# Kernel tuning notes

Measured on AMD Instinct MI355X. Metric: run time of the kernel, lower is better.

The kernel has to match this reference:

```python
import jax, jax.numpy as jnp
import numpy as np

H = 128   # hidden_dim
J = 24    # num_joints
L = 4     # num_layers
NH = 8    # attention heads
W = 120   # window
F = 256   # feedforward_size
D = 216   # input_dim (J * 9)
S = 60    # src len
T = 61    # tgt len (S+T-1 == W)
B = 2     # batch
HD = H // NH


def _ln(x, g, b, eps=1e-5):
    m = x.mean(-1, keepdims=True)
    v = ((x - m) ** 2).mean(-1, keepdims=True)
    return (x - m) / jnp.sqrt(v + eps) * g + b


def _mha(x, Wqkv, bqkv, Wo, bo, mask=None):
    # x: (seq, batch, H). torch MultiheadAttention with in_proj (3H,H), out_proj (H,H)
    s, bsz, _ = x.shape
    qkv = jnp.einsum('sbh,eh->sbe', x, Wqkv) + bqkv
    q, k, v = jnp.split(qkv, 3, axis=-1)
    q = q.reshape(s, bsz, NH, HD)
    k = k.reshape(s, bsz, NH, HD)
    v = v.reshape(s, bsz, NH, HD)
    scores = jnp.einsum('qbnd,kbnd->bnqk', q, k) * (1.0 / np.sqrt(HD))
    if mask is not None:
        scores = scores + mask
    a = jax.nn.softmax(scores, axis=-1)
    o = jnp.einsum('bnqk,kbnd->qbnd', a, v).reshape(s, bsz, H)
    return jnp.einsum('sbh,oh->sbo', o, Wo) + bo


def _make_pe(length, d):
    pos = np.arange(length)[:, None]
    div = np.exp(np.arange(0, d, 2) * (-np.log(10000.0) / d))
    pe = np.zeros((length, d), np.float32)
    pe[:, 0::2] = np.sin(pos * div)
    pe[:, 1::2] = np.cos(pos * div)
    return jnp.asarray(pe)


def setup_inputs() -> dict:
    key = jax.random.key(0)
    ks = jax.random.split(key, 16)
    def rn(i, shape, s=0.02):
        return jax.random.normal(ks[i], shape, dtype=jnp.float32) * s
    return {
        'src': rn(0, (B, S, D), 1.0),
        'tgt': rn(1, (B, T, D), 1.0),
        'Wemb': rn(2, (H * J, D)), 'bemb': jnp.zeros((H * J,), jnp.float32),
        'Wqkv_s': rn(3, (L, 3 * H, H)), 'bqkv_s': jnp.zeros((L, 3 * H), jnp.float32),
        'Wo_s': rn(4, (L, H, H)), 'bo_s': jnp.zeros((L, H), jnp.float32),
        'sn_g': jnp.ones((L, H), jnp.float32), 'sn_b': jnp.zeros((L, H), jnp.float32),
        'Wqkv_t': rn(5, (L, J, 3 * H, H)), 'bqkv_t': jnp.zeros((L, J, 3 * H), jnp.float32),
        'Wo_t': rn(6, (L, J, H, H)), 'bo_t': jnp.zeros((L, J, H), jnp.float32),
        'tn_g': jnp.ones((L, H), jnp.float32), 'tn_b': jnp.zeros((L, H), jnp.float32),
        'W1': rn(7, (L, F, H)), 'b1': jnp.zeros((L, F), jnp.float32),
        'W2': rn(8, (L, H, F)), 'b2': jnp.zeros((L, H), jnp.float32),
        'Wout': rn(9, (D // J, H)), 'bout': jnp.zeros((D // J,), jnp.float32),
    }


def _forward(src, tgt, Wemb, bemb, Wqkv_s, bqkv_s, Wo_s, bo_s, sn_g, sn_b,
             Wqkv_t, bqkv_t, Wo_t, bo_t, tn_g, tn_b, W1, b1, W2, b2, Wout, bout):
    src_ = src.swapaxes(0, 1)  # (S, B, D)
    tgt_ = tgt.swapaxes(0, 1)  # (T, B, D)
    concat = jnp.concatenate([src_, tgt_], axis=0)  # (W+1, B, D)
    total = concat.shape[0]
    max_len = total - 1  # == W
    emb = jnp.einsum('tbd,ed->tbe', concat, Wemb) + bemb
    emb = emb + _make_pe(total, H * J)[:, None, :]
    x0 = emb.reshape(total, concat.shape[1], J, H)
    # additive causal mask (original uses -inf; -1e9 is equivalent post-softmax)
    mask = jnp.asarray(np.where(np.tril(np.ones((W, W), bool)), 0.0, -1e9).astype(np.float32))
    tmha = jax.vmap(lambda xx, a, bb, c, dd: _mha(xx, a, bb, c, dd, mask))

    def layer(x, t, l):
        # spatial attention over joints at frame t
        sp = jnp.take(x, t, axis=0).transpose(1, 0, 2)  # (J, B, H)
        sa = _mha(sp, Wqkv_s[l], bqkv_s[l], Wo_s[l], bo_s[l])
        sp_out = _ln(sp + sa, sn_g[l], sn_b[l]).transpose(1, 0, 2)  # (B, J, H)
        # temporal attention per joint (distinct weights), causal over the window
        # since t < W always here, slice [max(0,t-W):max(t,W)] == [:W]
        temp = x[:W].transpose(2, 0, 1, 3)  # (J, W, B, H)
        ta = tmha(temp, Wqkv_t[l], bqkv_t[l], Wo_t[l], bo_t[l])
        tout = _ln(temp + ta, tn_g[l], tn_b[l]).transpose(1, 2, 0, 3)  # (W, B, J, H)
        tout = tout.at[t].add(sp_out)  # window_t = min(W-1, t) = t
        f = jax.nn.relu(jnp.einsum('wbjh,fh->wbjf', tout, W1[l]) + b1[l])
        f = 2.0 * f  # original: ffn = ffn + dropout(ffn); dropout is identity in eval
        return jnp.einsum('wbjf,hf->wbjh', f, W2[l]) + b2[l]

    def body(carry, t):
        x = x0
        for l in range(L):
            x = layer(x, t, l)
        proj = jnp.einsum('wbjh,oh->wbjo', x, Wout) + bout
        proj = proj.reshape(W, x.shape[1], D)
        out_t = jnp.take(proj, t, axis=0) + jnp.take(concat, t, axis=0)
        return carry, out_t

    _, outs = jax.lax.scan(body, None, jnp.arange(max_len))
    return outs.swapaxes(0, 1)  # (B, max_len, D)


def reference(src, tgt, Wemb, bemb, Wqkv_s, bqkv_s, Wo_s, bo_s, sn_g, sn_b,
              Wqkv_t, bqkv_t, Wo_t, bo_t, tn_g, tn_b, W1, b1, W2, b2, Wout, bout):
    return _forward(src, tgt, Wemb, bemb, Wqkv_s, bqkv_s, Wo_s, bo_s, sn_g, sn_b,
                    Wqkv_t, bqkv_t, Wo_t, bo_t, tn_g, tn_b, W1, b1, W2, b2, Wout, bout)
```

## Files before the change

kernel.cpp:

```cpp
#include <hip/hip_runtime.h>

#define TW 120
#define TB 2
#define TJ 24
#define TH 128
#define TNH 8
#define THD 16
#define TF 256
#define TD 216
#define TROWS (TW*TB*TJ)
#define TEMB (TJ*TH)
#define TBF 240
#define KPAD 256

#define QCH 60
#define LDT 136
#define SPAD (TH + 4)
#define HSEG (TW*THD)

typedef float f4 __attribute__((ext_vector_type(4)));
typedef short bf8 __attribute__((ext_vector_type(8)));
typedef short s4 __attribute__((ext_vector_type(4)));

__device__ __forceinline__ short f2bf(float x) {
    union { float f; unsigned u; } v; v.f = x;
    unsigned r = (v.u + 0x7FFFu + ((v.u >> 16) & 1u)) >> 16;
    return (short)r;
}

#define NW_QKV_S 196608
#define NW_O_S    65536
#define NW_QKV_T 4718592
#define NW_O_T   1572864
#define NW_1      131072
#define NW_2      131072
#define OFF_O_S   (NW_QKV_S)
#define OFF_QKV_T (OFF_O_S + NW_O_S)
#define OFF_O_T   (OFF_QKV_T + NW_QKV_T)
#define OFF_W1    (OFF_O_T + NW_O_T)
#define OFF_W2    (OFF_W1 + NW_1)
#define NW_TOT    (OFF_W2 + NW_2)
#define NB_CONV   (NW_TOT / 4 / 256)
#define NB_WEMB   (TEMB * KPAD / 4 / 256)
#define NB_CBUF   (TBF * KPAD / 4 / 256)

__global__ void convgather_kernel(const float* __restrict__ Wqkv_s, const float* __restrict__ Wo_s,
                                  const float* __restrict__ Wqkv_t, const float* __restrict__ Wo_t,
                                  const float* __restrict__ W1, const float* __restrict__ W2,
                                  short* __restrict__ dst,
                                  const float* __restrict__ Wemb, short* __restrict__ wembbf,
                                  const float* __restrict__ src, const float* __restrict__ tgt,
                                  short* __restrict__ cbufbf) {
    int bx = blockIdx.x, tid = threadIdx.x;
    if (bx < NB_CONV) {
        size_t i = ((size_t)bx * 256 + tid) * 4;
        const float* s; size_t off;
        if (i < NW_QKV_S)       { s = Wqkv_s; off = i; }
        else if (i < OFF_QKV_T) { s = Wo_s;   off = i - OFF_O_S; }
        else if (i < OFF_O_T)   { s = Wqkv_t; off = i - OFF_QKV_T; }
        else if (i < OFF_W1)    { s = Wo_t;   off = i - OFF_O_T; }
        else if (i < OFF_W2)    { s = W1;     off = i - OFF_W1; }
        else                    { s = W2;     off = i - OFF_W2; }
        f4 v = *(const f4*)(s + off);
        s4 o = { f2bf(v[0]), f2bf(v[1]), f2bf(v[2]), f2bf(v[3]) };
        *(s4*)(dst + i) = o;
    } else if (bx < NB_CONV + NB_WEMB) {
        int g = (bx - NB_CONV) * 256 + tid;
        int row = g >> 6;
        int colg = (g & 63) * 4;
        s4 o = {0, 0, 0, 0};
        if (colg < TD) {
            f4 v = *(const f4*)(Wemb + (size_t)row * TD + colg);
            o = { f2bf(v[0]), f2bf(v[1]), f2bf(v[2]), f2bf(v[3]) };
        }
        *(s4*)(wembbf + (size_t)row * KPAD + colg) = o;
    } else {
        int g = (bx - NB_CONV - NB_WEMB) * 256 + tid;
        int row = g >> 6;
        int colg = (g & 63) * 4;
        int b = row & 1, t = row >> 1;
        s4 o = {0, 0, 0, 0};
        if (colg < TD) {
            const float* sp = (t < 60) ? (src + ((size_t)b * 60 + t) * TD)
                                       : (tgt + ((size_t)b * 61 + (t - 60)) * TD);
            f4 v = *(const f4*)(sp + colg);
            o = { f2bf(v[0]), f2bf(v[1]), f2bf(v[2]), f2bf(v[3]) };
        }
        *(s4*)(cbufbf + (size_t)row * KPAD + colg) = o;
    }
}

__device__ __forceinline__ void stage_bf(short* Ds, const short* __restrict__ src,
                                         size_t rstride, int nrows, int tid) {
    int r = tid >> 2, s = (tid & 3) * 32;
    short* d = Ds + r * LDT + s;
    if (r < nrows) {
        const short* p = src + (size_t)r * rstride + s;
        *(bf8*)(d)      = *(const bf8*)(p);
        *(bf8*)(d + 8)  = *(const bf8*)(p + 8);
        *(bf8*)(d + 16) = *(const bf8*)(p + 16);
        *(bf8*)(d + 24) = *(const bf8*)(p + 24);
    } else {
        bf8 z = {0,0,0,0,0,0,0,0};
        *(bf8*)(d) = z; *(bf8*)(d+8) = z; *(bf8*)(d+16) = z; *(bf8*)(d+24) = z;
    }
}

__device__ __forceinline__ void mfma_tile64(const short* As, const short* Bs,
                                            int wave, int lane, f4 acc[2][2]) {
    int wm = wave >> 1, wn = wave & 1;
    int lrow = lane & 15, lk = (lane >> 4) * 8;
    #pragma unroll
    for (int ks = 0; ks < 4; ++ks) {
        bf8 a0 = *(const bf8*)&As[(wm*32      + lrow) * LDT + ks*32 + lk];
        bf8 a1 = *(const bf8*)&As[(wm*32 + 16 + lrow) * LDT + ks*32 + lk];
        bf8 b0 = *(const bf8*)&Bs[(wn*32      + lrow) * LDT + ks*32 + lk];
        bf8 b1 = *(const bf8*)&Bs[(wn*32 + 16 + lrow) * LDT + ks*32 + lk];
        acc[0][0] = __builtin_amdgcn_mfma_f32_16x16x32_bf16(a0, b0, acc[0][0], 0, 0, 0);
        acc[0][1] = __builtin_amdgcn_mfma_f32_16x16x32_bf16(a0, b1, acc[0][1], 0, 0, 0);
        acc[1][0] = __builtin_amdgcn_mfma_f32_16x16x32_bf16(a1, b0, acc[1][0], 0, 0, 0);
        acc[1][1] = __builtin_amdgcn_mfma_f32_16x16x32_bf16(a1, b1, acc[1][1], 0, 0, 0);
    }
}

__global__ __launch_bounds__(256) void mfma_embed_kernel(
        const short* __restrict__ cbufbf, const short* __restrict__ wembbf,
        const float* __restrict__ bemb, float* __restrict__ x0,
        short* __restrict__ x0bf, float* __restrict__ r0,
        short* __restrict__ r0bf) {
    __shared__ short As[64 * LDT], Bs[64 * LDT];
    int tid = threadIdx.x;
    int m0 = blockIdx.x * 64, n0 = blockIdx.y * 64;
    int mrem = TBF - m0; if (mrem > 64) mrem = 64;
    int wave = tid >> 6, lane = tid & 63;
    f4 acc[2][2] = {{{0,0,0,0},{0,0,0,0}},{{0,0,0,0},{0,0,0,0}}};
    #pragma unroll
    for (int kk = 0; kk < 2; ++kk) {
        stage_bf(As, cbufbf + (size_t)m0 * KPAD + kk * 128, KPAD, mrem, tid);
        stage_bf(Bs, wembbf + (size_t)n0 * KPAD + kk * 128, KPAD, 64, tid);
        __syncthreads();
        mfma_tile64(As, Bs, wave, lane, acc);
        __syncthreads();
    }
    int wm = wave >> 1, wn = wave & 1, lrow = lane & 15, gr = (lane >> 4) * 4;
    #pragma unroll
    for (int ni = 0; ni < 2; ++ni) {
        int col = n0 + wn*32 + ni*16 + lrow;
        float bv = bemb[col];
        float freq = expf((float)(col & ~1) * (-9.2103403719761836f / 3072.0f));
        float peodd = (col & 1) ? 1.f : 0.f;
        #pragma unroll
        for (int mi = 0; mi < 2; ++mi)
            #pragma unroll
            for (int rg = 0; rg < 4; ++rg) {
                int tr = wm*32 + mi*16 + gr + rg;
                if (tr < mrem) {
                    int grow = m0 + tr;
                    int t = grow >> 1;
                    float ang = (float)t * freq;
                    float pe = peodd ? cosf(ang) : sinf(ang);
                    float v = acc[mi][ni][rg] + bv + pe;
                    size_t off = (size_t)grow * TEMB + col;
                    x0[off] = v;
                    r0[off] = v;
                    short bvs = f2bf(v);
                    x0bf[off] = bvs;
                    r0bf[off] = bvs;
                }
            }
    }
}

__global__ __launch_bounds__(256) void mfma_qkvmega_kernel(
        const short* __restrict__ A2, const short* __restrict__ A3,
        const short* __restrict__ Wt, const short* __restrict__ Ws,
        const float* __restrict__ bt, const float* __restrict__ bs,
        float* __restrict__ Qp2, float* __restrict__ Kb2, float* __restrict__ Vb2,
        float* __restrict__ Qs_, float* __restrict__ Ks_, float* __restrict__ Vs_,
        float* __restrict__ Qt_, float* __restrict__ Kt_, float* __restrict__ Vt_,
        int p2n, int n0base) {
    __shared__ short As[64 * LDT], Bs[64 * LDT];
    int tid = threadIdx.x;
    int m0 = blockIdx.x * 64, j = blockIdx.z, yy = blockIdx.y;
    int mrem = TBF - m0; if (mrem > 64) mrem = 64;
    const short* Abf; const short* Wbf; const float* bias; int bofs, n0;
    float *dq, *dk, *dv;
    int headmajor;
    if (yy < p2n) {
        n0 = n0base + yy * 64;
        Abf = A2;
        Wbf = Wt + (size_t)j * 3 * TH * TH + (size_t)n0 * TH;
        bias = bt; bofs = j * 3 * TH;
        dq = Qp2; dk = Kb2; dv = Vb2;
        headmajor = 1;
    } else {
        int y2 = yy - p2n;
        int tmp = (y2 >= 6);
        n0 = (tmp ? y2 - 6 : y2) * 64;
        Abf = A3;
        if (tmp) { Wbf = Wt + (size_t)j * 3 * TH * TH + (size_t)n0 * TH; bias = bt; bofs = j * 3 * TH;
                   dq = Qt_; dk = Kt_; dv = Vt_; headmajor = 1; }
        else     { Wbf = Ws + (size_t)n0 * TH; bias = bs; bofs = 0;
                   dq = Qs_; dk = Ks_; dv = Vs_; headmajor = 0; }
    }
    stage_bf(As, Abf + (size_t)m0 * TEMB + j * TH, TEMB, mrem, tid);
    stage_bf(Bs, Wbf, TH, 64, tid);
    __syncthreads();
    int wave = tid >> 6, lane = tid & 63;
    f4 acc[2][2] = {{{0,0,0,0},{0,0,0,0}},{{0,0,0,0},{0,0,0,0}}};
    mfma_tile64(As, Bs, wave, lane, acc);
    int wm = wave >> 1, wn = wave & 1, lrow = lane & 15, gr = (lane >> 4) * 4;
    float* dst = (n0 < TH) ? dq : ((n0 < 2 * TH) ? dk : dv);
    int cb = n0 & (TH - 1);
    #pragma unroll
    for (int ni = 0; ni < 2; ++ni) {
        float bv = bias[bofs + n0 + wn*32 + ni*16 + lrow];
        int col = cb + wn*32 + ni*16 + lrow;
        #pragma unroll
        for (int mi = 0; mi < 2; ++mi)
            #pragma unroll
            for (int rg = 0; rg < 4; ++rg) {
                int tr = wm*32 + mi*16 + gr + rg;
                if (tr < mrem) {
                    int row = m0 + tr;
                    float v = acc[mi][ni][rg] + bv;
                    if (headmajor) {
                        int bb = row & 1, tt = row >> 1;
                        int hd = col >> 4, dd = col & 15;
                        dst[((size_t)((bb * TJ + j) * TNH + hd) * TW + tt) * THD + dd] = v;
                    } else {
                        dst[(size_t)(row * TJ + j) * TH + col] = v;
                    }
                }
            }
    }
}

__global__ __launch_bounds__(256) void attn_mega_kernel(
        const float* __restrict__ Qc_g, const float* __restrict__ Kc_g, const float* __restrict__ Vc_g,
        const float* __restrict__ Qs_g, const float* __restrict__ Ks_g, const float* __restrict__ Vs_g,
        const float* __restrict__ Qt_g, const float* __restrict__ Kt_g, const float* __restrict__ Vt_g,
        short* __restrict__ Oc, short* __restrict__ Os, short* __restrict__ Ot,
        int docausal) {
    __shared__ __align__(16) float smem[3 * TJ * SPAD];
    int bx = blockIdx.x;
    int tid = threadIdx.x;

    if (bx < 240) {
        float* Qs = smem;
        float* Ks = smem + TJ * SPAD;
        float* Vs = smem + 2 * TJ * SPAD;
        int b = bx & 1, t = bx >> 1;
        int base = (t * TB + b) * TJ;
        for (int i = tid; i < TJ * 32; i += 256) {
            int rr = i >> 5, c4 = i & 31;
            ((f4*)(Qs + rr * SPAD))[c4] = ((const f4*)(Qs_g + (size_t)(base + rr) * TH))[c4];
            ((f4*)(Ks + rr * SPAD))[c4] = ((const f4*)(Ks_g + (size_t)(base + rr) * TH))[c4];
            ((f4*)(Vs + rr * SPAD))[c4] = ((const f4*)(Vs_g + (size_t)(base + rr) * TH))[c4];
        }
        __syncthreads();
        if (tid >= 192) return;
        int qj = tid % TJ;
        int head = tid / TJ;
        int hb = head * THD;
        float qv[THD];
        #pragma unroll
        for (int u = 0; u < THD; ++u) qv[u] = Qs[qj * SPAD + hb + u];
        float sc[TJ];
        float m = -1e30f;
        #pragma unroll
        for (int k = 0; k < TJ; ++k) {
            float a = 0.f;
            #pragma unroll
            for (int u = 0; u < THD; ++u) a += qv[u] * Ks[k * SPAD + hb + u];
            sc[k] = a * 0.25f;
            m = fmaxf(m, sc[k]);
        }
        float sum = 0.f;
        #pragma unroll
        for (int k = 0; k < TJ; ++k) { sc[k] = __expf(sc[k] - m); sum += sc[k]; }
        float inv = 1.0f / sum;
        float o[THD];
        #pragma unroll
        for (int u = 0; u < THD; ++u) o[u] = 0.f;
        #pragma unroll
        for (int k = 0; k < TJ; ++k) {
            #pragma unroll
            for (int u = 0; u < THD; ++u) o[u] += sc[k] * Vs[k * SPAD + hb + u];
        }
        size_t off = (size_t)(base + qj) * TH + hb;
        #pragma unroll
        for (int u = 0; u < THD; ++u) Os[off + u] = f2bf(o[u] * inv);
        return;
    }

    int cx = bx - 240;
    int head = cx & 7;
    int j = (cx >> 3) % TJ;
    int b = (cx >> 3) / TJ;
    size_t base = (size_t)((b * TJ + j) * TNH + head) * HSEG;
    float* Kb = smem;
    float* Vb = smem + 1920;
    for (int i = tid; i < 480; i += 256) {
        ((f4*)Kb)[i] = ((const f4*)(Kc_g + base))[i];
        ((f4*)Vb)[i] = ((const f4*)(Vc_g + base))[i];
    }
    __syncthreads();
    int wave = tid >> 6, lane = tid & 63;
    int iscausal = (wave < 2);
    if (iscausal && !docausal) return;
    int qbase = (wave & 1) * 60;
    int act = (lane < 60);
    int q = qbase + (act ? lane : 59);
    const float* Qg = iscausal ? Qc_g : Qt_g;
    f4 Qr0 = *(const f4*)(Qg + base + (size_t)q * THD);
    f4 Qr1 = *(const f4*)(Qg + base + (size_t)q * THD + 4);
    f4 Qr2 = *(const f4*)(Qg + base + (size_t)q * THD + 8);
    f4 Qr3 = *(const f4*)(Qg + base + (size_t)q * THD + 12);
    f4 Ks0, Ks1, Ks2, Ks3, Vs0, Vs1, Vs2, Vs3;
    if (!iscausal) {
        Ks0 = *(const f4*)(Kt_g + base + (size_t)q * THD);
        Ks1 = *(const f4*)(Kt_g + base + (size_t)q * THD + 4);
        Ks2 = *(const f4*)(Kt_g + base + (size_t)q * THD + 8);
        Ks3 = *(const f4*)(Kt_g + base + (size_t)q * THD + 12);
        Vs0 = *(const f4*)(Vt_g + base + (size_t)q * THD);
        Vs1 = *(const f4*)(Vt_g + base + (size_t)q * THD + 4);
        Vs2 = *(const f4*)(Vt_g + base + (size_t)q * THD + 8);
        Vs3 = *(const f4*)(Vt_g + base + (size_t)q * THD + 12);
    }
    f4 a0 = {0,0,0,0}, a1 = {0,0,0,0}, a2 = {0,0,0,0}, a3 = {0,0,0,0};
    float sum = 0.f;
    int qc = iscausal ? q : (q - 1);
    int klim = qbase + 60;
    #pragma unroll 4
    for (int k = 0; k < klim; ++k) {
        const float* kr = Kb + k * 16;
        f4 d = Qr0 * ((const f4*)kr)[0] + Qr1 * ((const f4*)kr)[1]
             + Qr2 * ((const f4*)kr)[2] + Qr3 * ((const f4*)kr)[3];
        float s = (d[0] + d[1] + d[2] + d[3]) * 0.25f;
        float p = (k <= qc) ? __expf(s) : 0.f;
        sum += p;
        const float* vr = Vb + k * 16;
        a0 += p * ((const f4*)vr)[0];
        a1 += p * ((const f4*)vr)[1];
        a2 += p * ((const f4*)vr)[2];
        a3 += p * ((const f4*)vr)[3];
    }
    if (!iscausal) {
        f4 d = Qr0 * Ks0 + Qr1 * Ks1 + Qr2 * Ks2 + Qr3 * Ks3;
        float p = __expf((d[0] + d[1] + d[2] + d[3]) * 0.25f);
        sum += p;
        a0 += p * Vs0; a1 += p * Vs1; a2 += p * Vs2; a3 += p * Vs3;
    }
    if (act) {
        float inv = 1.0f / sum;
        short* O = iscausal ? Oc : Ot;
        size_t off = (size_t)((q * TB + b) * TJ + j) * TH + head * THD;
        s4 o0 = { f2bf(a0[0]*inv), f2bf(a0[1]*inv), f2bf(a0[2]*inv), f2bf(a0[3]*inv) };
        s4 o1 = { f2bf(a1[0]*inv), f2bf(a1[1]*inv), f2bf(a1[2]*inv), f2bf(a1[3]*inv) };
        s4 o2 = { f2bf(a2[0]*inv), f2bf(a2[1]*inv), f2bf(a2[2]*inv), f2bf(a2[3]*inv) };
        s4 o3 = { f2bf(a3[0]*inv), f2bf(a3[1]*inv), f2bf(a3[2]*inv), f2bf(a3[3]*inv) };
        *(s4*)(O + off)      = o0;
        *(s4*)(O + off + 4)  = o1;
        *(s4*)(O + off + 8)  = o2;
        *(s4*)(O + off + 12) = o3;
    }
}

__device__ __forceinline__ void oln_compute(
        const short* __restrict__ Abf, const short* __restrict__ Wbf,
        const float* __restrict__ bias, const float* __restrict__ resid,
        const float* __restrict__ g, const float* __restrict__ bln,
        int perJoint, int m0, int j,
        short* As, short* Bs, float* rsum, float* rsq, float* lnm, float* lnr,
        float o0[4], float o1[4]) {
    int tid = threadIdx.x;
    { int r = tid >> 4, s = (tid & 15) * 8;
      *(bf8*)&As[r * LDT + s] = *(const bf8*)(Abf + (size_t)(m0 + r) * TEMB + j * TH + s); }
    { int r = tid >> 1, s = (tid & 1) * 64;
      const short* p = Wbf + (perJoint ? (size_t)j * TH * TH : 0) + (size_t)r * TH + s;
      short* d = &Bs[r * LDT + s];
      #pragma unroll
      for (int cc = 0; cc < 64; cc += 8) *(bf8*)(d + cc) = *(const bf8*)(p + cc); }
    __syncthreads();
    int wave = tid >> 6, lane = tid & 63, lrow = lane & 15, lk = (lane >> 4) * 8, gr = (lane >> 4) * 4;
    f4 acc[2] = {{0,0,0,0},{0,0,0,0}};
    #pragma unroll
    for (int ks = 0; ks < 4; ++ks) {
        bf8 a  = *(const bf8*)&As[lrow * LDT + ks*32 + lk];
        bf8 b0 = *(const bf8*)&Bs[(wave*32      + lrow) * LDT + ks*32 + lk];
        bf8 b1 = *(const bf8*)&Bs[(wave*32 + 16 + lrow) * LDT + ks*32 + lk];
        acc[0] = __builtin_amdgcn_mfma_f32_16x16x32_bf16(a, b0, acc[0], 0, 0, 0);
        acc[1] = __builtin_amdgcn_mfma_f32_16x16x32_bf16(a, b1, acc[1], 0, 0, 0);
    }
    int col0 = wave*32 + lrow, col1 = col0 + 16;
    int bofs = perJoint ? j * TH : 0;
    float bv0 = bias[bofs + col0], bv1 = bias[bofs + col1];
    float v0[4], v1[4], sr_[4], sq_[4];
    #pragma unroll
    for (int rg = 0; rg < 4; ++rg) {
        size_t ro = (size_t)(m0 + gr + rg) * TEMB + j * TH;
        v0[rg] = acc[0][rg] + bv0 + resid[ro + col0];
        v1[rg] = acc[1][rg] + bv1 + resid[ro + col1];
        sr_[rg] = v0[rg] + v1[rg];
        sq_[rg] = v0[rg]*v0[rg] + v1[rg]*v1[rg];
    }
    #pragma unroll
    for (int o = 1; o < 16; o <<= 1) {
        #pragma unroll
        for (int rg = 0; rg < 4; ++rg) { sr_[rg] += __shfl_xor(sr_[rg], o); sq_[rg] += __shfl_xor(sq_[rg], o); }
    }
    if (lrow == 0) {
        #pragma unroll
        for (int rg = 0; rg < 4; ++rg) { rsum[wave*16 + gr + rg] = sr_[rg]; rsq[wave*16 + gr + rg] = sq_[rg]; }
    }
    __syncthreads();
    if (tid < 16) {
        float s = rsum[tid] + rsum[16 + tid] + rsum[32 + tid] + rsum[48 + tid];
        float q = rsq[tid] + rsq[16 + tid] + rsq[32 + tid] + rsq[48 + tid];
        float mean = s * (1.0f / TH);
        float var = q * (1.0f / TH) - mean * mean;
        lnm[tid] = mean; lnr[tid] = rsqrtf(var + 1e-5f);
    }
    __syncthreads();
    float g0 = g[col0], g1 = g[col1], l0 = bln[col0], l1 = bln[col1];
    #pragma unroll
    for (int rg = 0; rg < 4; ++rg) {
        int row = gr + rg;
        float mean = lnm[row], rs = lnr[row];
        o0[rg] = (v0[rg] - mean) * rs * g0 + l0;
        o1[rg] = (v1[rg] - mean) * rs * g1 + l1;
    }
}

__global__ __launch_bounds__(256) void mfma_olnfused_kernel(
        const short* __restrict__ A2, const short* __restrict__ Wt,
        const float* __restrict__ bt, const float* __restrict__ res2,
        const float* __restrict__ tg, const float* __restrict__ tl,
        short* __restrict__ Yb2,
        const short* __restrict__ A3s, const short* __restrict__ Ws,
        const float* __restrict__ bs, const short* __restrict__ A3t,
        const float* __restrict__ res3,
        const float* __restrict__ sg, const float* __restrict__ sl,
        short* __restrict__ Yb3, int np2) {
    __shared__ short As[16 * LDT];
    __shared__ short Bs[128 * LDT];
    __shared__ float rsum[64], rsq[64], lnm[16], lnr[16];
    int bx = blockIdx.x;
    int tid = threadIdx.x;
    int wave = tid >> 6, lane = tid & 63, lrow = lane & 15, gr = (lane >> 4) * 4;
    int col0 = wave*32 + lrow, col1 = col0 + 16;
    if (bx < np2) {
        int m0 = (bx % 15) * 16, j = bx / 15;
        float o0[4], o1[4];
        oln_compute(A2, Wt, bt, res2, tg, tl, 1, m0, j,
                    As, Bs, rsum, rsq, lnm, lnr, o0, o1);
        #pragma unroll
        for (int rg = 0; rg < 4; ++rg) {
            size_t ro = (size_t)(m0 + gr + rg) * TEMB + j * TH;
            Yb2[ro + col0] = f2bf(o0[rg]);
            Yb2[ro + col1] = f2bf(o1[rg]);
        }
    } else {
        int idx = bx - np2;
        int m0 = (idx % 15) * 16, j = idx / 15;
        float s0[4], s1[4], t0[4], t1[4];
        oln_compute(A3s, Ws, bs, res3, sg, sl, 0, m0, j,
                    As, Bs, rsum, rsq, lnm, lnr, s0, s1);
        __syncthreads();
        oln_compute(A3t, Wt, bt, res3, tg, tl, 1, m0, j,
                    As, Bs, rsum, rsq, lnm, lnr, t0, t1);
        #pragma unroll
        for (int rg = 0; rg < 4; ++rg) {
            size_t ro = (size_t)(m0 + gr + rg) * TEMB + j * TH;
            Yb3[ro + col0] = f2bf(t0[rg] + s0[rg]);
            Yb3[ro + col1] = f2bf(t1[rg] + s1[rg]);
        }
    }
}

__global__ __launch_bounds__(256) void mfma_ffn1_kernel(
        const short* __restrict__ Ybf, const short* __restrict__ W1bf,
        const float* __restrict__ b1, short* __restrict__ Fb) {
    __shared__ short As[64 * LDT], Bs[64 * LDT];
    int tid = threadIdx.x;
    int m0 = blockIdx.x * 64, n0 = blockIdx.y * 64;
    stage_bf(As, Ybf + (size_t)m0 * TH, TH, 64, tid);
    stage_bf(Bs, W1bf + (size_t)n0 * TH, TH, 64, tid);
    __syncthreads();
    int wave = tid >> 6, lane = tid & 63;
    f4 acc[2][2] = {{{0,0,0,0},{0,0,0,0}},{{0,0,0,0},{0,0,0,0}}};
    mfma_tile64(As, Bs, wave, lane, acc);
    int wm = wave >> 1, wn = wave & 1, lrow = lane & 15, gr = (lane >> 4) * 4;
    #pragma unroll
    for (int ni = 0; ni < 2; ++ni) {
        int col = n0 + wn*32 + ni*16 + lrow;
        float bv = b1[col];
        #pragma unroll
        for (int mi = 0; mi < 2; ++mi)
            #pragma unroll
            for (int rg = 0; rg < 4; ++rg) {
                int tr = wm*32 + mi*16 + gr + rg;
                float v = 2.0f * fmaxf(acc[mi][ni][rg] + bv, 0.0f);
                Fb[(size_t)(m0 + tr) * TF + col] = f2bf(v);
            }
    }
}

__global__ __launch_bounds__(256) void mfma_ffn2_kernel(
        const short* __restrict__ Fb, const short* __restrict__ W2bf,
        const float* __restrict__ b2, float* __restrict__ OutAf,
        short* __restrict__ OutAbf, float* __restrict__ OutBf,
        short* __restrict__ OutBbf, int splitrow) {
    __shared__ short As[64 * LDT], Bs[64 * LDT];
    int tid = threadIdx.x;
    int m0 = blockIdx.x * 64, n0 = blockIdx.y * 64;
    int wave = tid >> 6, lane = tid & 63;
    f4 acc[2][2] = {{{0,0,0,0},{0,0,0,0}},{{0,0,0,0},{0,0,0,0}}};
    #pragma unroll
    for (int kk = 0; kk < 2; ++kk) {
        stage_bf(As, Fb + (size_t)m0 * TF + kk * 128, TF, 64, tid);
        stage_bf(Bs, W2bf + (size_t)n0 * TF + kk * 128, TF, 64, tid);
        __syncthreads();
        mfma_tile64(As, Bs, wave, lane, acc);
        __syncthreads();
    }
    int wm = wave >> 1, wn = wave & 1, lrow = lane & 15, gr = (lane >> 4) * 4;
    #pragma unroll
    for (int ni = 0; ni < 2; ++ni) {
        int col = n0 + wn*32 + ni*16 + lrow;
        float bv = b2[col];
        #pragma unroll
        for (int mi = 0; mi < 2; ++mi)
            #pragma unroll
            for (int rg = 0; rg < 4; ++rg) {
                int tr = wm*32 + mi*16 + gr + rg;
                int row = m0 + tr;
                float v = acc[mi][ni][rg] + bv;
                if (row < splitrow) {
                    size_t off = (size_t)row * TH + col;
                    OutAf[off] = v; OutAbf[off] = f2bf(v);
                } else {
                    size_t off = (size_t)(row - splitrow) * TH + col;
                    OutBf[off] = v; OutBbf[off] = f2bf(v);
                }
            }
    }
}

__global__ void final_kernel(const float* __restrict__ r4, const float* __restrict__ Wout,
                             const float* __restrict__ bout, const float* __restrict__ src,
                             const float* __restrict__ tgt, float* __restrict__ out) {
    int idx = blockIdx.x * 256 + threadIdx.x;
    if (idx >= TB * TW * TD) return;
    int d = idx % TD;
    int t = (idx / TD) % TW;
    int b = idx / (TD * TW);
    int j = d / 9, o = d % 9;
    const float* rr = r4 + (size_t)((t * TB + b) * TJ + j) * TH;
    const float* wt = Wout + (size_t)o * TH;
    float acc = bout[o];
    #pragma unroll 4
    for (int h = 0; h < TH; ++h) acc += rr[h] * wt[h];
    float cv = (t < 60) ? src[((size_t)b * 60 + t) * TD + d]
                        : tgt[((size_t)b * 61 + (t - 60)) * TD + d];
    out[idx] = acc + cv;
}

extern "C" void kernel_launch(void* const* d_in, const int* in_sizes, int n_in,
                              void* d_out, int out_size, void* d_ws, size_t ws_size,
                              hipStream_t stream) {
    const float* src    = (const float*)d_in[0];
    const float* tgt    = (const float*)d_in[1];
    const float* Wemb   = (const float*)d_in[2];
    const float* bemb   = (const float*)d_in[3];
    const float* Wqkv_s = (const float*)d_in[4];
    const float* bqkv_s = (const float*)d_in[5];
    const float* Wo_s   = (const float*)d_in[6];
    const float* bo_s   = (const float*)d_in[7];
    const float* sn_g   = (const float*)d_in[8];
    const float* sn_b   = (const float*)d_in[9];
    const float* Wqkv_t = (const float*)d_in[10];
    const float* bqkv_t = (const float*)d_in[11];
    const float* Wo_t   = (const float*)d_in[12];
    const float* bo_t   = (const float*)d_in[13];
    const float* tn_g   = (const float*)d_in[14];
    const float* tn_b   = (const float*)d_in[15];
    const float* W1     = (const float*)d_in[16];
    const float* b1     = (const float*)d_in[17];
    const float* W2     = (const float*)d_in[18];
    const float* b2     = (const float*)d_in[19];
    const float* Wout   = (const float*)d_in[20];
    const float* bout   = (const float*)d_in[21];
    float* out = (float*)d_out;

    const size_t RH = (size_t)TROWS * TH;
    float* f = (float*)d_ws;
    float* x0    = f;
    float* Kbase = x0 + RH;
    float* Vbase = Kbase + 4 * RH;
    float* r     = Vbase + 4 * RH;
    float* Qp2   = r + RH;
    float* Qs    = Qp2 + RH;
    float* Ks    = Qs + RH;
    float* Vs    = Ks + RH;
    float* Qt    = Vs + RH;
    float* Kt    = Qt + RH;
    float* Vt    = Kt + RH;
    float* Bb0   = Vt + RH;
    float* Bb1   = Bb0 + RH;
    short* sbase   = (short*)(Bb1 + RH);
    short* x0bf    = sbase;
    short* rbf     = x0bf + RH;
    short* attnb_c = rbf + RH;
    short* attnb_s = attnb_c + RH;
    short* attnb_t = attnb_s + RH;
    short* yball   = attnb_t + RH;
    short* fball   = yball + 2 * RH;
    short* Bb0bf   = fball + 2 * (size_t)TROWS * TF;
    short* Bb1bf   = Bb0bf + RH;
    short* wbf     = Bb1bf + RH;
    short* wembbf  = wbf + NW_TOT;
    short* cbufbf  = wembbf + (size_t)TEMB * KPAD;

    const short* wqkvs_bf = wbf;
    const short* wos_bf   = wbf + OFF_O_S;
    const short* wqkvt_bf = wbf + OFF_QKV_T;
    const short* wot_bf   = wbf + OFF_O_T;
    const short* w1bf     = wbf + OFF_W1;
    const short* w2bf     = wbf + OFF_W2;

    convgather_kernel<<<NB_CONV + NB_WEMB + NB_CBUF, 256, 0, stream>>>(
        Wqkv_s, Wo_s, Wqkv_t, Wo_t, W1, W2, wbf,
        Wemb, wembbf, src, tgt, cbufbf);

    mfma_embed_kernel<<<dim3(4, 48), 256, 0, stream>>>(
        cbufbf, wembbf, bemb, x0, x0bf, r, rbf);

    const float* Binf = x0;
    const short* Binbf = x0bf;
    for (int l = 0; l < 4; ++l) {
        int p2n = (l < 3) ? 6 : 4;
        int n0base = (l < 3) ? 0 : 128;
        int np2 = (l < 3) ? 360 : 0;
        const short* wt_l = wqkvt_bf + (size_t)l * TJ * 3 * TH * TH;
        const short* ws_l = wqkvs_bf + (size_t)l * 3 * TH * TH;
        const float* bt_l = bqkv_t + (size_t)l * TJ * 3 * TH;
        const float* bs_l = bqkv_s + (size_t)l * 3 * TH;

        mfma_qkvmega_kernel<<<dim3(4, p2n + 12, 24), 256, 0, stream>>>(
            Binbf, rbf, wt_l, ws_l, bt_l, bs_l,
            Qp2, Kbase + l * RH, Vbase + l * RH,
            Qs, Ks, Vs, Qt, Kt, Vt, p2n, n0base);

        attn_mega_kernel<<<240 + 384, 256, 0, stream>>>(
            Qp2, Kbase + l * RH, Vbase + l * RH,
            Qs, Ks, Vs, Qt, Kt, Vt,
            attnb_c, attnb_s, attnb_t, (l < 3) ? 1 : 0);

        mfma_olnfused_kernel<<<np2 + 360, 256, 0, stream>>>(
            attnb_c, wot_bf + (size_t)l * TJ * TH * TH, bo_t + (size_t)l * TJ * TH,
            Binf, tn_g + l * TH, tn_b + l * TH, yball,
            attnb_s, wos_bf + (size_t)l * TH * TH, bo_s + (size_t)l * TH,
            attnb_t, r, sn_g + l * TH, sn_b + l * TH, yball + RH, np2);

        if (l < 3) {
            mfma_ffn1_kernel<<<dim3(180, 4), 256, 0, stream>>>(
                yball, w1bf + (size_t)l * TF * TH, b1 + l * TF, fball);
            float* Boutf = (l & 1) ? Bb1 : Bb0;
            short* Boutbf = (l & 1) ? Bb1bf : Bb0bf;
            mfma_ffn2_kernel<<<dim3(180, 2), 256, 0, stream>>>(
                fball, w2bf + (size_t)l * TH * TF, b2 + l * TH,
                Boutf, Boutbf, r, rbf, TROWS);
            Binf = Boutf; Binbf = Boutbf;
        } else {
            mfma_ffn1_kernel<<<dim3(90, 4), 256, 0, stream>>>(
                yball + RH, w1bf + (size_t)l * TF * TH, b1 + l * TF, fball);
            mfma_ffn2_kernel<<<dim3(90, 2), 256, 0, stream>>>(
                fball, w2bf + (size_t)l * TH * TF, b2 + l * TH,
                r, rbf, r, rbf, 0);
        }
    }

    final_kernel<<<(TB * TW * TD + 255) / 256, 256, 0, stream>>>(r, Wout, bout, src, tgt, out);
}
```

Baseline: 260.2 us.

## Fuse FFN up and down projections into one kernel via shared-memory intermediate

Merges the two FFN GEMM kernels into one kernel per 64-row tile. The ReLU-doubled hidden activations stay in LDS, one 128-column half at a time, and are consumed right away by the second GEMM. This removes one kernel launch per layer and the global write and re-read of the bf16 intermediate buffer. In exchange the grid shrinks from 720/360 blocks to 180/90, and each block runs its stages serially with more LDS per block, which reduces parallelism and occupancy.

```diff
diff --git a/kernel.cpp b/kernel.cpp
--- a/kernel.cpp
+++ b/kernel.cpp
@@ -479,73 +479,73 @@
     }
 }
 
-__global__ __launch_bounds__(256) void mfma_ffn1_kernel(
+__global__ __launch_bounds__(256) void mfma_ffnf_kernel(
         const short* __restrict__ Ybf, const short* __restrict__ W1bf,
-        const float* __restrict__ b1, short* __restrict__ Fb) {
-    __shared__ short As[64 * LDT], Bs[64 * LDT];
-    int tid = threadIdx.x;
-    int m0 = blockIdx.x * 64, n0 = blockIdx.y * 64;
-    stage_bf(As, Ybf + (size_t)m0 * TH, TH, 64, tid);
-    stage_bf(Bs, W1bf + (size_t)n0 * TH, TH, 64, tid);
-    __syncthreads();
-    int wave = tid >> 6, lane = tid & 63;
-    f4 acc[2][2] = {{{0,0,0,0},{0,0,0,0}},{{0,0,0,0},{0,0,0,0}}};
-    mfma_tile64(As, Bs, wave, lane, acc);
-    int wm = wave >> 1, wn = wave & 1, lrow = lane & 15, gr = (lane >> 4) * 4;
-    #pragma unroll
-    for (int ni = 0; ni < 2; ++ni) {
-        int col = n0 + wn*32 + ni*16 + lrow;
-        float bv = b1[col];
-        #pragma unroll
-        for (int mi = 0; mi < 2; ++mi)
-            #pragma unroll
-            for (int rg = 0; rg < 4; ++rg) {
-                int tr = wm*32 + mi*16 + gr + rg;
-                float v = 2.0f * fmaxf(acc[mi][ni][rg] + bv, 0.0f);
-                Fb[(size_t)(m0 + tr) * TF + col] = f2bf(v);
-            }
-    }
-}
-
-__global__ __launch_bounds__(256) void mfma_ffn2_kernel(
-        const short* __restrict__ Fb, const short* __restrict__ W2bf,
+        const float* __restrict__ b1, const short* __restrict__ W2bf,
         const float* __restrict__ b2, float* __restrict__ OutAf,
         short* __restrict__ OutAbf, float* __restrict__ OutBf,
         short* __restrict__ OutBbf, int splitrow) {
-    __shared__ short As[64 * LDT], Bs[64 * LDT];
+    __shared__ short As[64 * LDT], Bs[64 * LDT], Fs[64 * LDT];
     int tid = threadIdx.x;
-    int m0 = blockIdx.x * 64, n0 = blockIdx.y * 64;
+    int m0 = blockIdx.x * 64;
     int wave = tid >> 6, lane = tid & 63;
-    f4 acc[2][2] = {{{0,0,0,0},{0,0,0,0}},{{0,0,0,0},{0,0,0,0}}};
-    #pragma unroll
-    for (int kk = 0; kk < 2; ++kk) {
-        stage_bf(As, Fb + (size_t)m0 * TF + kk * 128, TF, 64, tid);
-        stage_bf(Bs, W2bf + (size_t)n0 * TF + kk * 128, TF, 64, tid);
-        __syncthreads();
-        mfma_tile64(As, Bs, wave, lane, acc);
-        __syncthreads();
-    }
     int wm = wave >> 1, wn = wave & 1, lrow = lane & 15, gr = (lane >> 4) * 4;
-    #pragma unroll
-    for (int ni = 0; ni < 2; ++ni) {
-        int col = n0 + wn*32 + ni*16 + lrow;
-        float bv = b2[col];
-        #pragma unroll
-        for (int mi = 0; mi < 2; ++mi)
+    stage_bf(As, Ybf + (size_t)m0 * TH, TH, 64, tid);
+    f4 acc2[2][2][2] = {};
+    #pragma unroll
+    for (int half = 0; half < 2; ++half) {
+        #pragma unroll
+        for (int sub = 0; sub < 2; ++sub) {
+            int nt = half * 2 + sub;
+            stage_bf(Bs, W1bf + (size_t)(nt * 64) * TH, TH, 64, tid);
+            __syncthreads();
+            f4 acc[2][2] = {{{0,0,0,0},{0,0,0,0}},{{0,0,0,0},{0,0,0,0}}};
+            mfma_tile64(As, Bs, wave, lane, acc);
             #pragma unroll
-            for (int rg = 0; rg < 4; ++rg) {
-                int tr = wm*32 + mi*16 + gr + rg;
-                int row = m0 + tr;
-                float v = acc[mi][ni][rg] + bv;
-                if (row < splitrow) {
-                    size_t off = (size_t)row * TH + col;
-                    OutAf[off] = v; OutAbf[off] = f2bf(v);
-                } else {
-                    size_t off = (size_t)(row - splitrow) * TH + col;
-                    OutBf[off] = v; OutBbf[off] = f2bf(v);
+            for (int ni = 0; ni < 2; ++ni) {
+                int colloc = wn*32 + ni*16 + lrow;
+                float bv = b1[nt*64 + colloc];
+                #pragma unroll
+                for (int mi = 0; mi < 2; ++mi)
+                    #pragma unroll
+                    for (int rg = 0; rg < 4; ++rg) {
+                        int tr = wm*32 + mi*16 + gr + rg;
+                        float v = 2.0f * fmaxf(acc[mi][ni][rg] + bv, 0.0f);
+                        Fs[tr * LDT + sub*64 + colloc] = f2bf(v);
+                    }
+            }
+            __syncthreads();
+        }
+        #pragma unroll
+        for (int nt2 = 0; nt2 < 2; ++nt2) {
+            stage_bf(Bs, W2bf + (size_t)(nt2 * 64) * TF + half * 128, TF, 64, tid);
+            __syncthreads();
+            mfma_tile64(Fs, Bs, wave, lane, acc2[nt2]);
+            __syncthreads();
+        }
+    }
+    #pragma unroll
+    for (int nt2 = 0; nt2 < 2; ++nt2)
+        #pragma unroll
+        for (int ni = 0; ni < 2; ++ni) {
+            int col = nt2*64 + wn*32 + ni*16 + lrow;
+            float bv = b2[col];
+            #pragma unroll
+            for (int mi = 0; mi < 2; ++mi)
+                #pragma unroll
+                for (int rg = 0; rg < 4; ++rg) {
+                    int tr = wm*32 + mi*16 + gr + rg;
+                    int row = m0 + tr;
+                    float v = acc2[nt2][mi][ni][rg] + bv;
+                    if (row < splitrow) {
+                        size_t off = (size_t)row * TH + col;
+                        OutAf[off] = v; OutAbf[off] = f2bf(v);
+                    } else {
+                        size_t off = (size_t)(row - splitrow) * TH + col;
+                        OutBf[off] = v; OutBbf[off] = f2bf(v);
+                    }
                 }
-            }
-    }
+        }
 }
 
 __global__ void final_kernel(const float* __restrict__ r4, const float* __restrict__ Wout,
@@ -665,19 +665,17 @@
             attnb_t, r, sn_g + l * TH, sn_b + l * TH, yball + RH, np2);
 
         if (l < 3) {
-            mfma_ffn1_kernel<<<dim3(180, 4), 256, 0, stream>>>(
-                yball, w1bf + (size_t)l * TF * TH, b1 + l * TF, fball);
             float* Boutf = (l & 1) ? Bb1 : Bb0;
             short* Boutbf = (l & 1) ? Bb1bf : Bb0bf;
-            mfma_ffn2_kernel<<<dim3(180, 2), 256, 0, stream>>>(
-                fball, w2bf + (size_t)l * TH * TF, b2 + l * TH,
+            mfma_ffnf_kernel<<<180, 256, 0, stream>>>(
+                yball, w1bf + (size_t)l * TF * TH, b1 + l * TF,
+                w2bf + (size_t)l * TH * TF, b2 + l * TH,
                 Boutf, Boutbf, r, rbf, TROWS);
             Binf = Boutf; Binbf = Boutbf;
         } else {
-            mfma_ffn1_kernel<<<dim3(90, 4), 256, 0, stream>>>(
-                yball + RH, w1bf + (size_t)l * TF * TH, b1 + l * TF, fball);
-            mfma_ffn2_kernel<<<dim3(90, 2), 256, 0, stream>>>(
-                fball, w2bf + (size_t)l * TH * TF, b2 + l * TH,
+            mfma_ffnf_kernel<<<90, 256, 0, stream>>>(
+                yball + RH, w1bf + (size_t)l * TF * TH, b1 + l * TF,
+                w2bf + (size_t)l * TH * TF, b2 + l * TH,
                 r, rbf, r, rbf, 0);
         }
     }
```

Result: no change. 264.2 us (+1.5%).

## Split attention key range across waves with shared-memory partial reduction

Applied to the files above, without the earlier changes.

The attention kernel now launches 512 threads per block. The upper query half is split across two waves, each covering 60 keys, so wave work is balanced instead of one wave looping over 120 keys. Partial accumulators and sums go through a shared-memory buffer and are merged after a block barrier. This shortens the critical path per block at the cost of an extra barrier, shared memory, and more threads, which may lower occupancy. The spatial branch leaves its extra threads idle.

```diff
diff --git a/kernel.cpp b/kernel.cpp
--- a/kernel.cpp
+++ b/kernel.cpp
@@ -236,7 +236,7 @@
     }
 }
 
-__global__ __launch_bounds__(256) void attn_mega_kernel(
+__global__ __launch_bounds__(512) void attn_mega_kernel(
         const float* __restrict__ Qc_g, const float* __restrict__ Kc_g, const float* __restrict__ Vc_g,
         const float* __restrict__ Qs_g, const float* __restrict__ Ks_g, const float* __restrict__ Vs_g,
         const float* __restrict__ Qt_g, const float* __restrict__ Kt_g, const float* __restrict__ Vt_g,
@@ -252,7 +252,7 @@
         float* Vs = smem + 2 * TJ * SPAD;
         int b = bx & 1, t = bx >> 1;
         int base = (t * TB + b) * TJ;
-        for (int i = tid; i < TJ * 32; i += 256) {
+        for (int i = tid; i < TJ * 32; i += 512) {
             int rr = i >> 5, c4 = i & 31;
             ((f4*)(Qs + rr * SPAD))[c4] = ((const f4*)(Qs_g + (size_t)(base + rr) * TH))[c4];
             ((f4*)(Ks + rr * SPAD))[c4] = ((const f4*)(Ks_g + (size_t)(base + rr) * TH))[c4];
@@ -301,58 +301,71 @@
     size_t base = (size_t)((b * TJ + j) * TNH + head) * HSEG;
     float* Kb = smem;
     float* Vb = smem + 1920;
-    for (int i = tid; i < 480; i += 256) {
+    float* pbuf = smem + 3840;
+    for (int i = tid; i < 480; i += 512) {
         ((f4*)Kb)[i] = ((const f4*)(Kc_g + base))[i];
         ((f4*)Vb)[i] = ((const f4*)(Vc_g + base))[i];
     }
     __syncthreads();
     int wave = tid >> 6, lane = tid & 63;
-    int iscausal = (wave < 2);
-    if (iscausal && !docausal) return;
-    int qbase = (wave & 1) * 60;
+    int iscausal = (wave < 3);
+    int active = (wave < 6) && (docausal || !iscausal);
+    int qhi = (wave == 1 || wave == 2 || wave == 4 || wave == 5);
     int act = (lane < 60);
-    int q = qbase + (act ? lane : 59);
-    const float* Qg = iscausal ? Qc_g : Qt_g;
-    f4 Qr0 = *(const f4*)(Qg + base + (size_t)q * THD);
-    f4 Qr1 = *(const f4*)(Qg + base + (size_t)q * THD + 4);
-    f4 Qr2 = *(const f4*)(Qg + base + (size_t)q * THD + 8);
-    f4 Qr3 = *(const f4*)(Qg + base + (size_t)q * THD + 12);
-    f4 Ks0, Ks1, Ks2, Ks3, Vs0, Vs1, Vs2, Vs3;
-    if (!iscausal) {
-        Ks0 = *(const f4*)(Kt_g + base + (size_t)q * THD);
-        Ks1 = *(const f4*)(Kt_g + base + (size_t)q * THD + 4);
-        Ks2 = *(const f4*)(Kt_g + base + (size_t)q * THD + 8);
-        Ks3 = *(const f4*)(Kt_g + base + (size_t)q * THD + 12);
-        Vs0 = *(const f4*)(Vt_g + base + (size_t)q * THD);
-        Vs1 = *(const f4*)(Vt_g + base + (size_t)q * THD + 4);
-        Vs2 = *(const f4*)(Vt_g + base + (size_t)q * THD + 8);
-        Vs3 = *(const f4*)(Vt_g + base + (size_t)q * THD + 12);
-    }
+    int q = (qhi ? 60 : 0) + (act ? lane : 59);
+    int k0 = (wave == 2 || wave == 5) ? 60 : 0;
+    int hasdiag = (wave == 3 || wave == 5);
     f4 a0 = {0,0,0,0}, a1 = {0,0,0,0}, a2 = {0,0,0,0}, a3 = {0,0,0,0};
     float sum = 0.f;
-    int qc = iscausal ? q : (q - 1);
-    int klim = qbase + 60;
-    #pragma unroll 4
-    for (int k = 0; k < klim; ++k) {
-        const float* kr = Kb + k * 16;
-        f4 d = Qr0 * ((const f4*)kr)[0] + Qr1 * ((const f4*)kr)[1]
-             + Qr2 * ((const f4*)kr)[2] + Qr3 * ((const f4*)kr)[3];
-        float s = (d[0] + d[1] + d[2] + d[3]) * 0.25f;
-        float p = (k <= qc) ? __expf(s) : 0.f;
-        sum += p;
-        const float* vr = Vb + k * 16;
-        a0 += p * ((const f4*)vr)[0];
-        a1 += p * ((const f4*)vr)[1];
-        a2 += p * ((const f4*)vr)[2];
-        a3 += p * ((const f4*)vr)[3];
-    }
-    if (!iscausal) {
-        f4 d = Qr0 * Ks0 + Qr1 * Ks1 + Qr2 * Ks2 + Qr3 * Ks3;
-        float p = __expf((d[0] + d[1] + d[2] + d[3]) * 0.25f);
-        sum += p;
-        a0 += p * Vs0; a1 += p * Vs1; a2 += p * Vs2; a3 += p * Vs3;
-    }
-    if (act) {
+    if (active) {
+        const float* Qg = iscausal ? Qc_g : Qt_g;
+        f4 Qr0 = *(const f4*)(Qg + base + (size_t)q * THD);
+        f4 Qr1 = *(const f4*)(Qg + base + (size_t)q * THD + 4);
+        f4 Qr2 = *(const f4*)(Qg + base + (size_t)q * THD + 8);
+        f4 Qr3 = *(const f4*)(Qg + base + (size_t)q * THD + 12);
+        int qc = iscausal ? q : (q - 1);
+        #pragma unroll 4
+        for (int k = k0; k < k0 + 60; ++k) {
+            const float* kr = Kb + k * 16;
+            f4 d = Qr0 * ((const f4*)kr)[0] + Qr1 * ((const f4*)kr)[1]
+                 + Qr2 * ((const f4*)kr)[2] + Qr3 * ((const f4*)kr)[3];
+            float s = (d[0] + d[1] + d[2] + d[3]) * 0.25f;
+            float p = (k <= qc) ? __expf(s) : 0.f;
+            sum += p;
+            const float* vr = Vb + k * 16;
+            a0 += p * ((const f4*)vr)[0];
+            a1 += p * ((const f4*)vr)[1];
+            a2 += p * ((const f4*)vr)[2];
+            a3 += p * ((const f4*)vr)[3];
+        }
+        if (hasdiag) {
+            f4 Ks0 = *(const f4*)(Kt_g + base + (size_t)q * THD);
+            f4 Ks1 = *(const f4*)(Kt_g + base + (size_t)q * THD + 4);
+            f4 Ks2 = *(const f4*)(Kt_g + base + (size_t)q * THD + 8);
+            f4 Ks3 = *(const f4*)(Kt_g + base + (size_t)q * THD + 12);
+            f4 Vd0 = *(const f4*)(Vt_g + base + (size_t)q * THD);
+            f4 Vd1 = *(const f4*)(Vt_g + base + (size_t)q * THD + 4);
+            f4 Vd2 = *(const f4*)(Vt_g + base + (size_t)q * THD + 8);
+            f4 Vd3 = *(const f4*)(Vt_g + base + (size_t)q * THD + 12);
+            f4 d = Qr0 * Ks0 + Qr1 * Ks1 + Qr2 * Ks2 + Qr3 * Ks3;
+            float p = __expf((d[0] + d[1] + d[2] + d[3]) * 0.25f);
+            sum += p;
+            a0 += p * Vd0; a1 += p * Vd1; a2 += p * Vd2; a3 += p * Vd3;
+        }
+    }
+    if (active && act && (wave == 1 || wave == 4)) {
+        float* p = pbuf + ((wave == 4 ? 60 : 0) + lane) * 20;
+        *(f4*)(p) = a0; *(f4*)(p + 4) = a1; *(f4*)(p + 8) = a2; *(f4*)(p + 12) = a3;
+        p[16] = sum;
+    }
+    __syncthreads();
+    if (active && act && (wave == 0 || wave == 2 || wave == 3 || wave == 5)) {
+        if (wave == 2 || wave == 5) {
+            const float* p = pbuf + ((wave == 5 ? 60 : 0) + lane) * 20;
+            a0 += *(const f4*)(p); a1 += *(const f4*)(p + 4);
+            a2 += *(const f4*)(p + 8); a3 += *(const f4*)(p + 12);
+            sum += p[16];
+        }
         float inv = 1.0f / sum;
         short* O = iscausal ? Oc : Ot;
         size_t off = (size_t)((q * TB + b) * TJ + j) * TH + head * THD;
@@ -653,7 +666,7 @@
             Qp2, Kbase + l * RH, Vbase + l * RH,
             Qs, Ks, Vs, Qt, Kt, Vt, p2n, n0base);
 
-        attn_mega_kernel<<<240 + 384, 256, 0, stream>>>(
+        attn_mega_kernel<<<240 + 384, 512, 0, stream>>>(
             Qp2, Kbase + l * RH, Vbase + l * RH,
             Qs, Ks, Vs, Qt, Kt, Vt,
             attnb_c, attnb_s, attnb_t, (l < 3) ? 1 : 0);
```

Result: faster. 250.4 us (-3.8%).
